# Kernel optimization log

Measured on AMD Instinct MI355X. Metric: run time of the kernel, lower is better.

The kernel has to match this reference:

```python
import jax, jax.numpy as jnp
import numpy as np

B, S, L, D, C_ENC, H = 8, 4096, 77, 1280, 2048, 20
DH = D // H          # 64
SCALE = DH ** -0.5


def setup_inputs() -> dict:
    key = jax.random.key(0)
    ks = jax.random.split(key, 8)
    return {
        "hidden_states": jax.random.normal(ks[0], (B, S, D), jnp.float32),
        "encoder_hidden_states": jax.random.normal(ks[1], (B, L, C_ENC), jnp.float32),
        "region_state": jax.random.uniform(ks[2], (B, S, L), jnp.float32),
        "Wq": jax.random.normal(ks[3], (D, D), jnp.float32) * 0.02,
        "Wk": jax.random.normal(ks[4], (C_ENC, D), jnp.float32) * 0.02,
        "Wv": jax.random.normal(ks[5], (C_ENC, D), jnp.float32) * 0.02,
        "Wo": jax.random.normal(ks[6], (D, D), jnp.float32) * 0.02,
        "bo": jnp.zeros((D,), jnp.float32),
        "sigma": jnp.ones((1,), jnp.float32) * 14.6,
    }


def reference(hidden_states, encoder_hidden_states, region_state, Wq, Wk, Wv, Wo, bo, sigma):
    # QKV projections (dense GEMMs)
    q = (hidden_states @ Wq).reshape(B, S, H, DH)            # [B,S,H,dh]
    k = (encoder_hidden_states @ Wk).reshape(B, L, H, DH)    # [B,L,H,dh]
    v = (encoder_hidden_states @ Wv).reshape(B, L, H, DH)
    # scaled attention scores (baddbmm with beta=0 == plain scaled matmul)
    scores = jnp.einsum('bshd,blhd->bhsl', q, k) * SCALE      # [B,H,S,L]
    # region-prompt bias: weight_func(w, sigma, qk) = w * log(1 + 0.1*sigma) * qk.max()
    # repeat_interleave over heads == broadcast over the head axis
    bias = region_state * (jnp.log1p(sigma[0] * 0.1) * scores.max())  # [B,S,L]
    scores = scores + bias[:, None, :, :]
    probs = jax.nn.softmax(scores, axis=-1)
    out = jnp.einsum('bhsl,blhd->bshd', probs, v).reshape(B, S, D)
    # output projection (to_out[0]); to_out[1] is dropout (identity at eval)
    return out @ Wo + bo
```

## Files before the change

### kernel.cpp

```cpp
#include <hip/hip_runtime.h>
#include <hip/hip_bf16.h>
#include <math.h>

#define NB 8
#define NS 4096
#define NL 77
#define NLP 80
#define NLPV 96
#define ND 1280
#define NC 2048
#define NH 20
#define NDH 64
#define QK_SCALE 0.125f

typedef __attribute__((ext_vector_type(4))) float f32x4;
typedef __attribute__((ext_vector_type(8))) short bf16x8;

static __device__ __forceinline__ void gload_lds16(const void* g, void* l) {
  __builtin_amdgcn_global_load_lds(
      (const __attribute__((address_space(1))) void*)g,
      (__attribute__((address_space(3))) void*)l, 16, 0, 0);
}

#define BAR() do { asm volatile("" ::: "memory"); __builtin_amdgcn_s_barrier(); asm volatile("" ::: "memory"); } while (0)
#define LGKM0() asm volatile("s_waitcnt lgkmcnt(0)" ::: "memory")

__global__ void cvt_bf16_kern(const float* __restrict__ in,
                              __hip_bfloat16* __restrict__ out, long n)
{
  long i = ((long)blockIdx.x * blockDim.x + threadIdx.x) * 4;
  long stride = (long)gridDim.x * blockDim.x * 4;
  for (; i < n; i += stride) {
    float4 v = *reinterpret_cast<const float4*>(in + i);
    union { __hip_bfloat16 h[4]; ushort4 u; } r;
    r.h[0] = __float2bfloat16(v.x);
    r.h[1] = __float2bfloat16(v.y);
    r.h[2] = __float2bfloat16(v.z);
    r.h[3] = __float2bfloat16(v.w);
    *reinterpret_cast<ushort4*>(out + i) = r.u;
  }
}

__global__ void transpose_bf16_kern(const float* __restrict__ in,
                                    __hip_bfloat16* __restrict__ out,
                                    int rows, int cols)
{
  __shared__ float t[32][33];
  int c0 = blockIdx.x * 32, r0 = blockIdx.y * 32;
  int tx = threadIdx.x, ty = threadIdx.y;
  for (int i = ty; i < 32; i += 8) {
    int r = r0 + i, c = c0 + tx;
    t[i][tx] = (r < rows && c < cols) ? in[(long)r * cols + c] : 0.f;
  }
  __syncthreads();
  for (int i = ty; i < 32; i += 8) {
    int oc = c0 + i, orr = r0 + tx;
    if (oc < cols && orr < rows)
      out[(long)oc * rows + orr] = __float2bfloat16(t[tx][i]);
  }
}

__global__ __launch_bounds__(256)
void gemm_bt_kern(const __hip_bfloat16* __restrict__ A,
                  const __hip_bfloat16* __restrict__ Bt,
                  void* __restrict__ C, const float* __restrict__ bias,
                  int M, int N, int K, int mode)
{
  __shared__ __align__(16) __hip_bfloat16 As[128 * 32];
  __shared__ __align__(16) __hip_bfloat16 Bs[128 * 32];
  const int t = threadIdx.x;
  const int lane = t & 63;
  const int w = t >> 6;
  const int wm = w >> 1, wn = w & 1;
  const int lr = lane & 15, hi = lane >> 4, lk = hi * 8;
  const long m0 = (long)blockIdx.x * 128;
  const long n0 = (long)blockIdx.y * 128;

  f32x4 acc[4][4];
#pragma unroll
  for (int mi = 0; mi < 4; ++mi)
#pragma unroll
    for (int ni = 0; ni < 4; ++ni) acc[mi][ni] = {0.f, 0.f, 0.f, 0.f};

  for (int k0 = 0; k0 < K; k0 += 32) {
    __syncthreads();
#pragma unroll
    for (int rnd = 0; rnd < 2; ++rnd) {
      int idx = rnd * 256 + t;
      int row = idx >> 2, kpp = (idx & 3) * 8;
      long arow = m0 + row; if (arow >= M) arow = M - 1;
      gload_lds16(A + arow * K + k0 + kpp, (void*)(As + idx * 8));
      long brow = n0 + row;
      gload_lds16(Bt + brow * K + k0 + kpp, (void*)(Bs + idx * 8));
    }
    __syncthreads();

    bf16x8 af[4], bfr[4];
#pragma unroll
    for (int i = 0; i < 4; ++i) {
      af[i]  = *reinterpret_cast<const bf16x8*>(As + (wm * 64 + i * 16 + lr) * 32 + lk);
      bfr[i] = *reinterpret_cast<const bf16x8*>(Bs + (wn * 64 + i * 16 + lr) * 32 + lk);
    }
#pragma unroll
    for (int mi = 0; mi < 4; ++mi)
#pragma unroll
      for (int ni = 0; ni < 4; ++ni)
        acc[mi][ni] = __builtin_amdgcn_mfma_f32_16x16x32_bf16(af[mi], bfr[ni], acc[mi][ni], 0, 0, 0);
  }

#pragma unroll
  for (int mi = 0; mi < 4; ++mi) {
#pragma unroll
    for (int r = 0; r < 4; ++r) {
      long row = m0 + wm * 64 + mi * 16 + hi * 4 + r;
      if (row < M) {
#pragma unroll
        for (int ni = 0; ni < 4; ++ni) {
          long col = n0 + wn * 64 + ni * 16 + lr;
          if (mode == 0)
            ((__hip_bfloat16*)C)[row * N + col] = __float2bfloat16(acc[mi][ni][r]);
          else
            ((float*)C)[row * N + col] = acc[mi][ni][r] + bias[col];
        }
      }
    }
  }
}

__global__ __launch_bounds__(256, 2)
void gemm_qmax_kern(const __hip_bfloat16* __restrict__ A,
                    const __hip_bfloat16* __restrict__ Bt,
                    __hip_bfloat16* __restrict__ C,
                    const __hip_bfloat16* __restrict__ kp,
                    float* __restrict__ bmax,
                    int M, int N, int K)
{
  __shared__ __align__(16) __hip_bfloat16 sm[32768];
  char* smc = (char*)sm;

  const int t = threadIdx.x, lane = t & 63, w = t >> 6;
  const int wm = w >> 1, wn = w & 1;
  const int lr = lane & 15, hi = lane >> 4;
  const int sw = lr & 7;

  int nwg = gridDim.x;
  int cpx = nwg >> 3;
  int swz = (blockIdx.x & 7) * cpx + (blockIdx.x >> 3);
  int nxt = N >> 7;
  int mt = swz / nxt, ntile = swz - mt * nxt;
  const long m0 = (long)mt * 128, n0 = (long)ntile * 128;

  const int srow  = t >> 3;
  const int skoff = ((t & 7) ^ (srow & 7)) * 8;
  const int sdst  = t * 16;

  f32x4 acc[4][4];
#pragma unroll
  for (int mi = 0; mi < 4; ++mi)
#pragma unroll
    for (int ni = 0; ni < 4; ++ni) acc[mi][ni] = {0.f, 0.f, 0.f, 0.f};

  auto stageA = [&](int b, int kt) {
#pragma unroll
    for (int c = 0; c < 4; ++c)
      gload_lds16(A + (m0 + c * 32 + srow) * (long)K + kt * 64 + skoff,
                  (void*)(smc + b * 16384 + c * 4096 + sdst));
  };
  auto stageB = [&](int b, int kt) {
#pragma unroll
    for (int c = 0; c < 4; ++c)
      gload_lds16(Bt + (n0 + c * 32 + srow) * (long)K + kt * 64 + skoff,
                  (void*)(smc + 32768 + b * 16384 + c * 4096 + sdst));
  };

  const int NT = K >> 6;
  stageA(0, 0); stageB(0, 0);
  stageA(1, 1); stageB(1, 1);
  asm volatile("s_waitcnt vmcnt(8)" ::: "memory");
  BAR();

  for (int t2 = 0; t2 < NT; ++t2) {
    const int b = t2 & 1;
    const char* pa = smc + b * 16384;
    const char* pb = smc + 32768 + b * 16384;
    const bool pf = (t2 + 2 < NT);

    bf16x8 af[4][2], bfr[4][2];
#pragma unroll
    for (int mi = 0; mi < 4; ++mi) {
      int row = wm * 64 + mi * 16 + lr;
#pragma unroll
      for (int kk = 0; kk < 2; ++kk)
        af[mi][kk] = *reinterpret_cast<const bf16x8*>(
            pa + row * 128 + ((((kk * 4 + hi) ^ sw)) << 4));
    }
#pragma unroll
    for (int ni = 0; ni < 4; ++ni) {
      int row = wn * 64 + ni * 16 + lr;
#pragma unroll
      for (int kk = 0; kk < 2; ++kk)
        bfr[ni][kk] = *reinterpret_cast<const bf16x8*>(
            pb + row * 128 + ((((kk * 4 + hi) ^ sw)) << 4));
    }
    __builtin_amdgcn_s_setprio(1);
#pragma unroll
    for (int mi = 0; mi < 4; ++mi)
#pragma unroll
      for (int ni = 0; ni < 4; ++ni) {
        acc[mi][ni] = __builtin_amdgcn_mfma_f32_16x16x32_bf16(af[mi][0], bfr[ni][0], acc[mi][ni], 0, 0, 0);
        acc[mi][ni] = __builtin_amdgcn_mfma_f32_16x16x32_bf16(af[mi][1], bfr[ni][1], acc[mi][ni], 0, 0, 0);
      }
    __builtin_amdgcn_s_setprio(0);

    LGKM0();
    BAR();
    if (pf) { stageA(b, t2 + 2); stageB(b, t2 + 2); }
    if (pf) { asm volatile("s_waitcnt vmcnt(8)" ::: "memory"); }
    else    { asm volatile("s_waitcnt vmcnt(0)" ::: "memory"); }
    BAR();
  }

  __hip_bfloat16* qsl = (__hip_bfloat16*)smc;
#pragma unroll
  for (int mi = 0; mi < 4; ++mi)
#pragma unroll
    for (int r = 0; r < 4; ++r) {
      int rowl = wm * 64 + mi * 16 + hi * 4 + r;
      long row = m0 + rowl;
#pragma unroll
      for (int ni = 0; ni < 4; ++ni) {
        int col = wn * 64 + ni * 16 + lr;
        __hip_bfloat16 v = __float2bfloat16(acc[mi][ni][r]);
        C[row * N + n0 + col] = v;
        int bw = (col >> 3) ^ (rowl & 7);
        qsl[rowl * 128 + (bw << 3) + (col & 7)] = v;
      }
    }
  LGKM0();
  BAR();
  const int bb = (int)(m0 >> 12);
  float mx = -1e30f;
#pragma unroll
  for (int hh = 0; hh < 2; ++hh) {
    const int h = (int)(n0 >> 6) + hh;
    bf16x8 bk0[5], bk1[5];
#pragma unroll
    for (int lt = 0; lt < 5; ++lt) {
      const __hip_bfloat16* Kr = kp + ((long)(bb * NLP + lt * 16 + lr)) * ND + h * NDH + hi * 8;
      bk0[lt] = *reinterpret_cast<const bf16x8*>(Kr);
      bk1[lt] = *reinterpret_cast<const bf16x8*>(Kr + 32);
    }
#pragma unroll
    for (int su = 0; su < 2; ++su) {
      int qrow = (w * 2 + su) * 16 + lr;
      int bi0 = (hh * 8 + hi)     ^ sw;
      int bi1 = (hh * 8 + 4 + hi) ^ sw;
      bf16x8 aq0 = *reinterpret_cast<const bf16x8*>(qsl + qrow * 128 + (bi0 << 3));
      bf16x8 aq1 = *reinterpret_cast<const bf16x8*>(qsl + qrow * 128 + (bi1 << 3));
#pragma unroll
      for (int lt = 0; lt < 5; ++lt) {
        f32x4 sc = {0.f, 0.f, 0.f, 0.f};
        sc = __builtin_amdgcn_mfma_f32_16x16x32_bf16(aq0, bk0[lt], sc, 0, 0, 0);
        sc = __builtin_amdgcn_mfma_f32_16x16x32_bf16(aq1, bk1[lt], sc, 0, 0, 0);
        if ((lt < 4) || (lr < 13)) {
#pragma unroll
          for (int r = 0; r < 4; ++r) mx = fmaxf(mx, sc[r]);
        }
      }
    }
  }
#pragma unroll
  for (int k = 32; k >= 1; k >>= 1) mx = fmaxf(mx, __shfl_xor(mx, k));
  float* wmx = (float*)(smc + 32768);
  if (lane == 0) wmx[w] = mx;
  LGKM0();
  BAR();
  if (t == 0) {
    float mm = fmaxf(fmaxf(wmx[0], wmx[1]), fmaxf(wmx[2], wmx[3]));
    bmax[blockIdx.x] = mm * QK_SCALE;
  }
}

__global__ __launch_bounds__(256, 2)
void gemm_out_kern(const __hip_bfloat16* __restrict__ A,
                   const __hip_bfloat16* __restrict__ Bt,
                   float* __restrict__ C, const float* __restrict__ bias,
                   int M, int N, int K)
{
  __shared__ __align__(16) __hip_bfloat16 sm[32768];
  char* smc = (char*)sm;

  const int t = threadIdx.x, lane = t & 63, w = t >> 6;
  const int wm = w >> 1, wn = w & 1;
  const int lr = lane & 15, hi = lane >> 4;
  const int sw = lr & 7;

  int nwg = gridDim.x;
  int cpx = nwg >> 3;
  int swz = (blockIdx.x & 7) * cpx + (blockIdx.x >> 3);
  int nxt = N >> 7;
  int mt = swz / nxt, ntile = swz - mt * nxt;
  const long m0 = (long)mt * 128, n0 = (long)ntile * 128;

  const int srow  = t >> 3;
  const int skoff = ((t & 7) ^ (srow & 7)) * 8;
  const int sdst  = t * 16;

  f32x4 acc[4][4];
#pragma unroll
  for (int mi = 0; mi < 4; ++mi)
#pragma unroll
    for (int ni = 0; ni < 4; ++ni) acc[mi][ni] = {0.f, 0.f, 0.f, 0.f};

  auto stageA = [&](int b, int kt) {
#pragma unroll
    for (int c = 0; c < 4; ++c)
      gload_lds16(A + (m0 + c * 32 + srow) * (long)K + kt * 64 + skoff,
                  (void*)(smc + b * 16384 + c * 4096 + sdst));
  };
  auto stageB = [&](int b, int kt) {
#pragma unroll
    for (int c = 0; c < 4; ++c)
      gload_lds16(Bt + (n0 + c * 32 + srow) * (long)K + kt * 64 + skoff,
                  (void*)(smc + 32768 + b * 16384 + c * 4096 + sdst));
  };

  const int NT = K >> 6;
  stageA(0, 0); stageB(0, 0);
  stageA(1, 1); stageB(1, 1);
  asm volatile("s_waitcnt vmcnt(8)" ::: "memory");
  BAR();

  for (int t2 = 0; t2 < NT; ++t2) {
    const int b = t2 & 1;
    const char* pa = smc + b * 16384;
    const char* pb = smc + 32768 + b * 16384;
    const bool pf = (t2 + 2 < NT);

    bf16x8 af[4][2], bfr[4][2];
#pragma unroll
    for (int mi = 0; mi < 4; ++mi) {
      int row = wm * 64 + mi * 16 + lr;
#pragma unroll
      for (int kk = 0; kk < 2; ++kk)
        af[mi][kk] = *reinterpret_cast<const bf16x8*>(
            pa + row * 128 + ((((kk * 4 + hi) ^ sw)) << 4));
    }
#pragma unroll
    for (int ni = 0; ni < 4; ++ni) {
      int row = wn * 64 + ni * 16 + lr;
#pragma unroll
      for (int kk = 0; kk < 2; ++kk)
        bfr[ni][kk] = *reinterpret_cast<const bf16x8*>(
            pb + row * 128 + ((((kk * 4 + hi) ^ sw)) << 4));
    }
    __builtin_amdgcn_s_setprio(1);
#pragma unroll
    for (int mi = 0; mi < 4; ++mi)
#pragma unroll
      for (int ni = 0; ni < 4; ++ni) {
        acc[mi][ni] = __builtin_amdgcn_mfma_f32_16x16x32_bf16(af[mi][0], bfr[ni][0], acc[mi][ni], 0, 0, 0);
        acc[mi][ni] = __builtin_amdgcn_mfma_f32_16x16x32_bf16(af[mi][1], bfr[ni][1], acc[mi][ni], 0, 0, 0);
      }
    __builtin_amdgcn_s_setprio(0);

    LGKM0();
    BAR();
    if (pf) { stageA(b, t2 + 2); stageB(b, t2 + 2); }
    if (pf) { asm volatile("s_waitcnt vmcnt(8)" ::: "memory"); }
    else    { asm volatile("s_waitcnt vmcnt(0)" ::: "memory"); }
    BAR();
  }

  float bv[4];
#pragma unroll
  for (int ni = 0; ni < 4; ++ni) bv[ni] = bias[n0 + wn * 64 + ni * 16 + lr];
#pragma unroll
  for (int mi = 0; mi < 4; ++mi)
#pragma unroll
    for (int r = 0; r < 4; ++r) {
      long row = m0 + wm * 64 + mi * 16 + hi * 4 + r;
#pragma unroll
      for (int ni = 0; ni < 4; ++ni) {
        long col = n0 + wn * 64 + ni * 16 + lr;
        C[row * N + col] = acc[mi][ni][r] + bv[ni];
      }
    }
}

__global__ void repack_kv_kern(const __hip_bfloat16* __restrict__ kvc,
                               __hip_bfloat16* __restrict__ kp,
                               __hip_bfloat16* __restrict__ vt)
{
  int idx = blockIdx.x * 256 + threadIdx.x;
  const __hip_bfloat16 z = __float2bfloat16(0.f);
  if (idx < NB * NLP * ND) {
    int d = idx % ND;
    int l = (idx / ND) % NLP;
    int b = idx / (ND * NLP);
    kp[idx] = (l < NL) ? kvc[((long)(b * NL + l)) * 2560 + d] : z;
  }
  if (idx < NB * NH * NDH * NLPV) {
    int l  = idx % NLPV;
    int dh = (idx / NLPV) % NDH;
    int h  = (idx / (NLPV * NDH)) % NH;
    int b  = idx / (NLPV * NDH * NH);
    vt[idx] = (l < NL) ? kvc[((long)(b * NL + l)) * 2560 + ND + h * NDH + dh] : z;
  }
}

__global__ void reduce_max_kern(const float* __restrict__ bm, int n,
                                const float* __restrict__ sigma,
                                float* __restrict__ cb)
{
  __shared__ float sm[256];
  float m = -1e30f;
  for (int i = threadIdx.x; i < n; i += 256) m = fmaxf(m, bm[i]);
  sm[threadIdx.x] = m;
  __syncthreads();
  for (int s = 128; s > 0; s >>= 1) {
    if (threadIdx.x < (unsigned)s) sm[threadIdx.x] = fmaxf(sm[threadIdx.x], sm[threadIdx.x + s]);
    __syncthreads();
  }
  if (threadIdx.x == 0) cb[0] = log1pf(sigma[0] * 0.1f) * sm[0];
}

__global__ __launch_bounds__(256)
void attn_kern(const __hip_bfloat16* __restrict__ qb,
               const __hip_bfloat16* __restrict__ kp,
               const __hip_bfloat16* __restrict__ vt,
               const float* __restrict__ rs,
               const float* __restrict__ cb,
               __hip_bfloat16* __restrict__ ao_out)
{
  __shared__ __align__(16) float rsl[64][80];
  __shared__ __align__(16) __hip_bfloat16 pl[4][16][NLPV];
  int t = threadIdx.x, lane = t & 63, wi = t >> 6;
  int b = blockIdx.y;
  int s0 = blockIdx.x * 64;
  int lr = lane & 15, hi = lane >> 4, lk = hi * 8;
  const float c = cb[0];

  for (int i = t; i < 64 * NL; i += 256) {
    int rr = i / NL, cc = i - rr * NL;
    rsl[rr][cc] = rs[((long)(b * NS + s0 + rr)) * NL + cc] * c;
  }
#pragma unroll
  for (int r = 0; r < 4; ++r)
    pl[wi][hi * 4 + r][80 + lr] = __float2bfloat16(0.f);
  __syncthreads();

  const int rw = wi * 16;
  const __hip_bfloat16* Qrow = qb + ((long)(b * NS + s0 + rw + lr)) * ND;
  const __hip_bfloat16* Krow = kp + ((long)(b * NLP + lr)) * ND;

  for (int h = 0; h < NH; ++h) {
    const __hip_bfloat16* Qp = Qrow + h * NDH + lk;
    bf16x8 aq0 = *reinterpret_cast<const bf16x8*>(Qp);
    bf16x8 aq1 = *reinterpret_cast<const bf16x8*>(Qp + 32);

    f32x4 sc[5];
#pragma unroll
    for (int lt = 0; lt < 5; ++lt) {
      const __hip_bfloat16* Kr = Krow + (long)lt * 16 * ND + h * NDH + lk;
      bf16x8 bk0 = *reinterpret_cast<const bf16x8*>(Kr);
      bf16x8 bk1 = *reinterpret_cast<const bf16x8*>(Kr + 32);
      f32x4 z = {0.f, 0.f, 0.f, 0.f};
      z = __builtin_amdgcn_mfma_f32_16x16x32_bf16(aq0, bk0, z, 0, 0, 0);
      sc[lt] = __builtin_amdgcn_mfma_f32_16x16x32_bf16(aq1, bk1, z, 0, 0, 0);
    }

    float sv[5][4];
    float pm[4] = {-1e30f, -1e30f, -1e30f, -1e30f};
#pragma unroll
    for (int lt = 0; lt < 5; ++lt) {
      int l = lt * 16 + lr;
#pragma unroll
      for (int r = 0; r < 4; ++r) {
        if (l < NL) {
          float v = sc[lt][r] * QK_SCALE + rsl[rw + hi * 4 + r][l];
          sv[lt][r] = v;
          pm[r] = fmaxf(pm[r], v);
        } else {
          sv[lt][r] = -1e30f;
        }
      }
    }
#pragma unroll
    for (int r = 0; r < 4; ++r)
#pragma unroll
      for (int k = 8; k >= 1; k >>= 1) pm[r] = fmaxf(pm[r], __shfl_xor(pm[r], k));

    float p[5][4];
    float psum[4] = {0.f, 0.f, 0.f, 0.f};
#pragma unroll
    for (int lt = 0; lt < 5; ++lt) {
      int l = lt * 16 + lr;
#pragma unroll
      for (int r = 0; r < 4; ++r) {
        float e = (l < NL) ? __expf(sv[lt][r] - pm[r]) : 0.f;
        p[lt][r] = e;
        psum[r] += e;
      }
    }
#pragma unroll
    for (int r = 0; r < 4; ++r)
#pragma unroll
      for (int k = 8; k >= 1; k >>= 1) psum[r] += __shfl_xor(psum[r], k);
    float rinv[4];
#pragma unroll
    for (int r = 0; r < 4; ++r) rinv[r] = 1.f / psum[r];

    LGKM0();

#pragma unroll
    for (int lt = 0; lt < 5; ++lt)
#pragma unroll
      for (int r = 0; r < 4; ++r)
        pl[wi][hi * 4 + r][lt * 16 + lr] = __float2bfloat16(p[lt][r]);

    LGKM0();

    f32x4 ao[4];
#pragma unroll
    for (int nt = 0; nt < 4; ++nt) ao[nt] = {0.f, 0.f, 0.f, 0.f};
    const __hip_bfloat16* Vb = vt + ((long)((b * NH + h) * NDH)) * NLPV;
#pragma unroll
    for (int ks = 0; ks < 3; ++ks) {
      bf16x8 pa = *reinterpret_cast<const bf16x8*>(&pl[wi][lr][ks * 32 + lk]);
#pragma unroll
      for (int nt = 0; nt < 4; ++nt) {
        bf16x8 bv = *reinterpret_cast<const bf16x8*>(Vb + ((long)(nt * 16 + lr)) * NLPV + ks * 32 + lk);
        ao[nt] = __builtin_amdgcn_mfma_f32_16x16x32_bf16(pa, bv, ao[nt], 0, 0, 0);
      }
    }

#pragma unroll
    for (int nt = 0; nt < 4; ++nt)
#pragma unroll
      for (int r = 0; r < 4; ++r) {
        int srow = s0 + rw + hi * 4 + r;
        ao_out[((long)(b * NS + srow)) * ND + h * NDH + nt * 16 + lr] =
            __float2bfloat16(ao[nt][r] * rinv[r]);
      }
  }
}

extern "C" void kernel_launch(void* const* d_in, const int* in_sizes, int n_in,
                              void* d_out, int out_size, void* d_ws, size_t ws_size,
                              hipStream_t stream)
{
  const float* hs    = (const float*)d_in[0];
  const float* ehs   = (const float*)d_in[1];
  const float* rs    = (const float*)d_in[2];
  const float* Wq    = (const float*)d_in[3];
  const float* Wk    = (const float*)d_in[4];
  const float* Wv    = (const float*)d_in[5];
  const float* Wo    = (const float*)d_in[6];
  const float* bo    = (const float*)d_in[7];
  const float* sigma = (const float*)d_in[8];
  float* out = (float*)d_out;

  char* ws = (char*)d_ws;
  size_t off = 0;
  auto alloc = [&](size_t bytes) {
    void* p = ws + off;
    off = (off + bytes + 255) & ~(size_t)255;
    return p;
  };
  __hip_bfloat16* hsb  = (__hip_bfloat16*)alloc((size_t)NB * NS * ND * 2);
  __hip_bfloat16* qb   = (__hip_bfloat16*)alloc((size_t)NB * NS * ND * 2);
  __hip_bfloat16* wqt  = (__hip_bfloat16*)alloc((size_t)ND * ND * 2);
  __hip_bfloat16* wkvt = (__hip_bfloat16*)alloc((size_t)2560 * NC * 2);
  __hip_bfloat16* wot  = (__hip_bfloat16*)alloc((size_t)ND * ND * 2);
  __hip_bfloat16* ehsb = (__hip_bfloat16*)alloc((size_t)NB * NL * NC * 2);
  __hip_bfloat16* kvc  = (__hip_bfloat16*)alloc((size_t)NB * NL * 2560 * 2);
  __hip_bfloat16* kp   = (__hip_bfloat16*)alloc((size_t)NB * NLP * ND * 2);
  __hip_bfloat16* vt   = (__hip_bfloat16*)alloc((size_t)NB * NH * NDH * NLPV * 2);
  float* bmax = (float*)alloc(10240 * 4);
  float* cb   = (float*)alloc(256);

  cvt_bf16_kern<<<2048, 256, 0, stream>>>(hs, hsb, (long)NB * NS * ND);
  cvt_bf16_kern<<<512, 256, 0, stream>>>(ehs, ehsb, (long)NB * NL * NC);

  transpose_bf16_kern<<<dim3(40, 40), dim3(32, 8), 0, stream>>>(Wq, wqt, ND, ND);
  transpose_bf16_kern<<<dim3(40, 64), dim3(32, 8), 0, stream>>>(Wk, wkvt, NC, ND);
  transpose_bf16_kern<<<dim3(40, 64), dim3(32, 8), 0, stream>>>(Wv, wkvt + (size_t)ND * NC, NC, ND);
  transpose_bf16_kern<<<dim3(40, 40), dim3(32, 8), 0, stream>>>(Wo, wot, ND, ND);

  gemm_bt_kern<<<dim3(5, 20), 256, 0, stream>>>(ehsb, wkvt, kvc, nullptr, NB * NL, 2560, NC, 0);
  repack_kv_kern<<<3840, 256, 0, stream>>>(kvc, kp, vt);

  gemm_qmax_kern<<<2560, 256, 0, stream>>>(hsb, wqt, qb, kp, bmax, NB * NS, ND, ND);

  reduce_max_kern<<<1, 256, 0, stream>>>(bmax, 2560, sigma, cb);

  attn_kern<<<dim3(NS / 64, NB), 256, 0, stream>>>(qb, kp, vt, rs, cb, hsb);

  gemm_out_kern<<<2560, 256, 0, stream>>>(hsb, wot, out, bo, NB * NS, ND, ND);
}
```

Baseline: 484.5 us.

## Fuse prep kernels, write K/V directly from GEMM, halve GEMM K-tile for occupancy

The six conversion and transpose launches are merged into one prep kernel. The KV GEMM epilogue now writes straight into the padded K and transposed V layouts, which removes the intermediate buffer and the repack kernel; padding comes from two memsets instead. The Q and output GEMMs drop from a 64 to a 32 K-tile with an unswizzled LDS layout, halving shared memory so launch bounds can request 4 blocks per SIMD instead of 2. The risks are more loop iterations and barriers per GEMM, possible LDS bank conflicts from the simpler layout, and register pressure at the higher occupancy.

Measured after the change: 634.4 us. 1.31x slower.

```diff
diff --git a/kernel.cpp b/kernel.cpp
--- a/kernel.cpp
+++ b/kernel.cpp
@@ -25,46 +25,61 @@
 #define BAR() do { asm volatile("" ::: "memory"); __builtin_amdgcn_s_barrier(); asm volatile("" ::: "memory"); } while (0)
 #define LGKM0() asm volatile("s_waitcnt lgkmcnt(0)" ::: "memory")
 
-__global__ void cvt_bf16_kern(const float* __restrict__ in,
-                              __hip_bfloat16* __restrict__ out, long n)
-{
-  long i = ((long)blockIdx.x * blockDim.x + threadIdx.x) * 4;
-  long stride = (long)gridDim.x * blockDim.x * 4;
-  for (; i < n; i += stride) {
-    float4 v = *reinterpret_cast<const float4*>(in + i);
-    union { __hip_bfloat16 h[4]; ushort4 u; } r;
-    r.h[0] = __float2bfloat16(v.x);
-    r.h[1] = __float2bfloat16(v.y);
-    r.h[2] = __float2bfloat16(v.z);
-    r.h[3] = __float2bfloat16(v.w);
-    *reinterpret_cast<ushort4*>(out + i) = r.u;
-  }
-}
-
-__global__ void transpose_bf16_kern(const float* __restrict__ in,
-                                    __hip_bfloat16* __restrict__ out,
-                                    int rows, int cols)
-{
-  __shared__ float t[32][33];
-  int c0 = blockIdx.x * 32, r0 = blockIdx.y * 32;
-  int tx = threadIdx.x, ty = threadIdx.y;
+__global__ __launch_bounds__(256)
+void prep_kern(const float* __restrict__ hs,  __hip_bfloat16* __restrict__ hsb,
+               const float* __restrict__ ehs, __hip_bfloat16* __restrict__ ehsb,
+               const float* __restrict__ Wq,  __hip_bfloat16* __restrict__ wqt,
+               const float* __restrict__ Wk,  const float* __restrict__ Wv,
+               __hip_bfloat16* __restrict__ wkvt,
+               const float* __restrict__ Wo,  __hip_bfloat16* __restrict__ wot)
+{
+  const int bid = blockIdx.x, t = threadIdx.x;
+  if (bid < 2560) {
+    const float* in; __hip_bfloat16* outp; long n; long i; long stride;
+    if (bid < 2048) {
+      in = hs; outp = hsb; n = (long)NB * NS * ND;
+      i = ((long)bid * 256 + t) * 4; stride = 2048L * 256 * 4;
+    } else {
+      in = ehs; outp = ehsb; n = (long)NB * NL * NC;
+      i = ((long)(bid - 2048) * 256 + t) * 4; stride = 512L * 256 * 4;
+    }
+    for (; i < n; i += stride) {
+      float4 v = *reinterpret_cast<const float4*>(in + i);
+      union { __hip_bfloat16 h[4]; ushort4 u; } r;
+      r.h[0] = __float2bfloat16(v.x);
+      r.h[1] = __float2bfloat16(v.y);
+      r.h[2] = __float2bfloat16(v.z);
+      r.h[3] = __float2bfloat16(v.w);
+      *reinterpret_cast<ushort4*>(outp + i) = r.u;
+    }
+    return;
+  }
+  __shared__ float tl[32][33];
+  const float* in; __hip_bfloat16* outp; int rows, cols, idx;
+  if (bid < 4160)      { idx = bid - 2560; in = Wq; outp = wqt; rows = 1280; cols = 1280; }
+  else if (bid < 6720) { idx = bid - 4160; in = Wk; outp = wkvt; rows = 2048; cols = 1280; }
+  else if (bid < 9280) { idx = bid - 6720; in = Wv; outp = wkvt + (size_t)ND * NC; rows = 2048; cols = 1280; }
+  else                 { idx = bid - 9280; in = Wo; outp = wot; rows = 1280; cols = 1280; }
+  int c0 = (idx % 40) * 32, r0 = (idx / 40) * 32;
+  int tx = t & 31, ty = t >> 5;
   for (int i = ty; i < 32; i += 8) {
     int r = r0 + i, c = c0 + tx;
-    t[i][tx] = (r < rows && c < cols) ? in[(long)r * cols + c] : 0.f;
+    tl[i][tx] = (r < rows && c < cols) ? in[(long)r * cols + c] : 0.f;
   }
   __syncthreads();
   for (int i = ty; i < 32; i += 8) {
     int oc = c0 + i, orr = r0 + tx;
     if (oc < cols && orr < rows)
-      out[(long)oc * rows + orr] = __float2bfloat16(t[tx][i]);
+      outp[(long)oc * rows + orr] = __float2bfloat16(tl[tx][i]);
   }
 }
 
 __global__ __launch_bounds__(256)
-void gemm_bt_kern(const __hip_bfloat16* __restrict__ A,
+void gemm_kv_kern(const __hip_bfloat16* __restrict__ A,
                   const __hip_bfloat16* __restrict__ Bt,
-                  void* __restrict__ C, const float* __restrict__ bias,
-                  int M, int N, int K, int mode)
+                  __hip_bfloat16* __restrict__ kp,
+                  __hip_bfloat16* __restrict__ vt,
+                  int M, int N, int K)
 {
   __shared__ __align__(16) __hip_bfloat16 As[128 * 32];
   __shared__ __align__(16) __hip_bfloat16 Bs[128 * 32];
@@ -114,20 +129,24 @@
     for (int r = 0; r < 4; ++r) {
       long row = m0 + wm * 64 + mi * 16 + hi * 4 + r;
       if (row < M) {
+        int b = (int)(row / NL), l = (int)(row - (long)b * NL);
 #pragma unroll
         for (int ni = 0; ni < 4; ++ni) {
           long col = n0 + wn * 64 + ni * 16 + lr;
-          if (mode == 0)
-            ((__hip_bfloat16*)C)[row * N + col] = __float2bfloat16(acc[mi][ni][r]);
-          else
-            ((float*)C)[row * N + col] = acc[mi][ni][r] + bias[col];
+          __hip_bfloat16 v = __float2bfloat16(acc[mi][ni][r]);
+          if (col < ND) {
+            kp[((long)(b * NLP + l)) * ND + col] = v;
+          } else {
+            int c2 = (int)(col - ND);
+            vt[(((long)(b * NH + (c2 >> 6))) * NDH + (c2 & 63)) * NLPV + l] = v;
+          }
         }
       }
     }
   }
 }
 
-__global__ __launch_bounds__(256, 2)
+__global__ __launch_bounds__(256, 4)
 void gemm_qmax_kern(const __hip_bfloat16* __restrict__ A,
                     const __hip_bfloat16* __restrict__ Bt,
                     __hip_bfloat16* __restrict__ C,
@@ -135,7 +154,8 @@
                     float* __restrict__ bmax,
                     int M, int N, int K)
 {
-  __shared__ __align__(16) __hip_bfloat16 sm[32768];
+  __shared__ __align__(16) __hip_bfloat16 sm[16384];
+  __shared__ float wmx[4];
   char* smc = (char*)sm;
 
   const int t = threadIdx.x, lane = t & 63, w = t >> 6;
@@ -150,9 +170,8 @@
   int mt = swz / nxt, ntile = swz - mt * nxt;
   const long m0 = (long)mt * 128, n0 = (long)ntile * 128;
 
-  const int srow  = t >> 3;
-  const int skoff = ((t & 7) ^ (srow & 7)) * 8;
-  const int sdst  = t * 16;
+  const int g_row = w * 16 + lr;
+  const int g_k   = hi * 8;
 
   f32x4 acc[4][4];
 #pragma unroll
@@ -162,60 +181,49 @@
 
   auto stageA = [&](int b, int kt) {
 #pragma unroll
-    for (int c = 0; c < 4; ++c)
-      gload_lds16(A + (m0 + c * 32 + srow) * (long)K + kt * 64 + skoff,
-                  (void*)(smc + b * 16384 + c * 4096 + sdst));
+    for (int c = 0; c < 2; ++c)
+      gload_lds16(A + (m0 + c * 64 + g_row) * (long)K + kt * 32 + g_k,
+                  (void*)(smc + b * 8192 + c * 4096 + t * 16));
   };
   auto stageB = [&](int b, int kt) {
 #pragma unroll
-    for (int c = 0; c < 4; ++c)
-      gload_lds16(Bt + (n0 + c * 32 + srow) * (long)K + kt * 64 + skoff,
-                  (void*)(smc + 32768 + b * 16384 + c * 4096 + sdst));
+    for (int c = 0; c < 2; ++c)
+      gload_lds16(Bt + (n0 + c * 64 + g_row) * (long)K + kt * 32 + g_k,
+                  (void*)(smc + 16384 + b * 8192 + c * 4096 + t * 16));
   };
 
-  const int NT = K >> 6;
+  const int NT = K >> 5;
   stageA(0, 0); stageB(0, 0);
   stageA(1, 1); stageB(1, 1);
-  asm volatile("s_waitcnt vmcnt(8)" ::: "memory");
+  asm volatile("s_waitcnt vmcnt(4)" ::: "memory");
   BAR();
 
   for (int t2 = 0; t2 < NT; ++t2) {
     const int b = t2 & 1;
-    const char* pa = smc + b * 16384;
-    const char* pb = smc + 32768 + b * 16384;
+    const char* pa = smc + b * 8192;
+    const char* pb = smc + 16384 + b * 8192;
     const bool pf = (t2 + 2 < NT);
 
-    bf16x8 af[4][2], bfr[4][2];
-#pragma unroll
-    for (int mi = 0; mi < 4; ++mi) {
-      int row = wm * 64 + mi * 16 + lr;
-#pragma unroll
-      for (int kk = 0; kk < 2; ++kk)
-        af[mi][kk] = *reinterpret_cast<const bf16x8*>(
-            pa + row * 128 + ((((kk * 4 + hi) ^ sw)) << 4));
-    }
-#pragma unroll
-    for (int ni = 0; ni < 4; ++ni) {
-      int row = wn * 64 + ni * 16 + lr;
-#pragma unroll
-      for (int kk = 0; kk < 2; ++kk)
-        bfr[ni][kk] = *reinterpret_cast<const bf16x8*>(
-            pb + row * 128 + ((((kk * 4 + hi) ^ sw)) << 4));
-    }
+    bf16x8 af[4], bfr[4];
+#pragma unroll
+    for (int mi = 0; mi < 4; ++mi)
+      af[mi] = *reinterpret_cast<const bf16x8*>(pa + (wm * 4 + mi) * 1024 + hi * 256 + lr * 16);
+#pragma unroll
+    for (int ni = 0; ni < 4; ++ni)
+      bfr[ni] = *reinterpret_cast<const bf16x8*>(pb + (wn * 4 + ni) * 1024 + hi * 256 + lr * 16);
+
     __builtin_amdgcn_s_setprio(1);
 #pragma unroll
     for (int mi = 0; mi < 4; ++mi)
 #pragma unroll
-      for (int ni = 0; ni < 4; ++ni) {
-        acc[mi][ni] = __builtin_amdgcn_mfma_f32_16x16x32_bf16(af[mi][0], bfr[ni][0], acc[mi][ni], 0, 0, 0);
-        acc[mi][ni] = __builtin_amdgcn_mfma_f32_16x16x32_bf16(af[mi][1], bfr[ni][1], acc[mi][ni], 0, 0, 0);
-      }
+      for (int ni = 0; ni < 4; ++ni)
+        acc[mi][ni] = __builtin_amdgcn_mfma_f32_16x16x32_bf16(af[mi], bfr[ni], acc[mi][ni], 0, 0, 0);
     __builtin_amdgcn_s_setprio(0);
 
     LGKM0();
     BAR();
     if (pf) { stageA(b, t2 + 2); stageB(b, t2 + 2); }
-    if (pf) { asm volatile("s_waitcnt vmcnt(8)" ::: "memory"); }
+    if (pf) { asm volatile("s_waitcnt vmcnt(4)" ::: "memory"); }
     else    { asm volatile("s_waitcnt vmcnt(0)" ::: "memory"); }
     BAR();
   }
@@ -271,7 +279,6 @@
   }
 #pragma unroll
   for (int k = 32; k >= 1; k >>= 1) mx = fmaxf(mx, __shfl_xor(mx, k));
-  float* wmx = (float*)(smc + 32768);
   if (lane == 0) wmx[w] = mx;
   LGKM0();
   BAR();
@@ -281,19 +288,18 @@
   }
 }
 
-__global__ __launch_bounds__(256, 2)
+__global__ __launch_bounds__(256, 4)
 void gemm_out_kern(const __hip_bfloat16* __restrict__ A,
                    const __hip_bfloat16* __restrict__ Bt,
                    float* __restrict__ C, const float* __restrict__ bias,
                    int M, int N, int K)
 {
-  __shared__ __align__(16) __hip_bfloat16 sm[32768];
+  __shared__ __align__(16) __hip_bfloat16 sm[16384];
   char* smc = (char*)sm;
 
   const int t = threadIdx.x, lane = t & 63, w = t >> 6;
   const int wm = w >> 1, wn = w & 1;
   const int lr = lane & 15, hi = lane >> 4;
-  const int sw = lr & 7;
 
   int nwg = gridDim.x;
   int cpx = nwg >> 3;
@@ -302,9 +308,8 @@
   int mt = swz / nxt, ntile = swz - mt * nxt;
   const long m0 = (long)mt * 128, n0 = (long)ntile * 128;
 
-  const int srow  = t >> 3;
-  const int skoff = ((t & 7) ^ (srow & 7)) * 8;
-  const int sdst  = t * 16;
+  const int g_row = w * 16 + lr;
+  const int g_k   = hi * 8;
 
   f32x4 acc[4][4];
 #pragma unroll
@@ -314,60 +319,49 @@
 
   auto stageA = [&](int b, int kt) {
 #pragma unroll
-    for (int c = 0; c < 4; ++c)
-      gload_lds16(A + (m0 + c * 32 + srow) * (long)K + kt * 64 + skoff,
-                  (void*)(smc + b * 16384 + c * 4096 + sdst));
+    for (int c = 0; c < 2; ++c)
+      gload_lds16(A + (m0 + c * 64 + g_row) * (long)K + kt * 32 + g_k,
+                  (void*)(smc + b * 8192 + c * 4096 + t * 16));
   };
   auto stageB = [&](int b, int kt) {
 #pragma unroll
-    for (int c = 0; c < 4; ++c)
-      gload_lds16(Bt + (n0 + c * 32 + srow) * (long)K + kt * 64 + skoff,
-                  (void*)(smc + 32768 + b * 16384 + c * 4096 + sdst));
+    for (int c = 0; c < 2; ++c)
+      gload_lds16(Bt + (n0 + c * 64 + g_row) * (long)K + kt * 32 + g_k,
+                  (void*)(smc + 16384 + b * 8192 + c * 4096 + t * 16));
   };
 
-  const int NT = K >> 6;
+  const int NT = K >> 5;
   stageA(0, 0); stageB(0, 0);
   stageA(1, 1); stageB(1, 1);
-  asm volatile("s_waitcnt vmcnt(8)" ::: "memory");
+  asm volatile("s_waitcnt vmcnt(4)" ::: "memory");
   BAR();
 
   for (int t2 = 0; t2 < NT; ++t2) {
     const int b = t2 & 1;
-    const char* pa = smc + b * 16384;
-    const char* pb = smc + 32768 + b * 16384;
+    const char* pa = smc + b * 8192;
+    const char* pb = smc + 16384 + b * 8192;
     const bool pf = (t2 + 2 < NT);
 
-    bf16x8 af[4][2], bfr[4][2];
-#pragma unroll
-    for (int mi = 0; mi < 4; ++mi) {
-      int row = wm * 64 + mi * 16 + lr;
-#pragma unroll
-      for (int kk = 0; kk < 2; ++kk)
-        af[mi][kk] = *reinterpret_cast<const bf16x8*>(
-            pa + row * 128 + ((((kk * 4 + hi) ^ sw)) << 4));
-    }
-#pragma unroll
-    for (int ni = 0; ni < 4; ++ni) {
-      int row = wn * 64 + ni * 16 + lr;
-#pragma unroll
-      for (int kk = 0; kk < 2; ++kk)
-        bfr[ni][kk] = *reinterpret_cast<const bf16x8*>(
-            pb + row * 128 + ((((kk * 4 + hi) ^ sw)) << 4));
-    }
+    bf16x8 af[4], bfr[4];
+#pragma unroll
+    for (int mi = 0; mi < 4; ++mi)
+      af[mi] = *reinterpret_cast<const bf16x8*>(pa + (wm * 4 + mi) * 1024 + hi * 256 + lr * 16);
+#pragma unroll
+    for (int ni = 0; ni < 4; ++ni)
+      bfr[ni] = *reinterpret_cast<const bf16x8*>(pb + (wn * 4 + ni) * 1024 + hi * 256 + lr * 16);
+
     __builtin_amdgcn_s_setprio(1);
 #pragma unroll
     for (int mi = 0; mi < 4; ++mi)
 #pragma unroll
-      for (int ni = 0; ni < 4; ++ni) {
-        acc[mi][ni] = __builtin_amdgcn_mfma_f32_16x16x32_bf16(af[mi][0], bfr[ni][0], acc[mi][ni], 0, 0, 0);
-        acc[mi][ni] = __builtin_amdgcn_mfma_f32_16x16x32_bf16(af[mi][1], bfr[ni][1], acc[mi][ni], 0, 0, 0);
-      }
+      for (int ni = 0; ni < 4; ++ni)
+        acc[mi][ni] = __builtin_amdgcn_mfma_f32_16x16x32_bf16(af[mi], bfr[ni], acc[mi][ni], 0, 0, 0);
     __builtin_amdgcn_s_setprio(0);
 
     LGKM0();
     BAR();
     if (pf) { stageA(b, t2 + 2); stageB(b, t2 + 2); }
-    if (pf) { asm volatile("s_waitcnt vmcnt(8)" ::: "memory"); }
+    if (pf) { asm volatile("s_waitcnt vmcnt(4)" ::: "memory"); }
     else    { asm volatile("s_waitcnt vmcnt(0)" ::: "memory"); }
     BAR();
   }
@@ -386,27 +380,6 @@
         C[row * N + col] = acc[mi][ni][r] + bv[ni];
       }
     }
-}
-
-__global__ void repack_kv_kern(const __hip_bfloat16* __restrict__ kvc,
-                               __hip_bfloat16* __restrict__ kp,
-                               __hip_bfloat16* __restrict__ vt)
-{
-  int idx = blockIdx.x * 256 + threadIdx.x;
-  const __hip_bfloat16 z = __float2bfloat16(0.f);
-  if (idx < NB * NLP * ND) {
-    int d = idx % ND;
-    int l = (idx / ND) % NLP;
-    int b = idx / (ND * NLP);
-    kp[idx] = (l < NL) ? kvc[((long)(b * NL + l)) * 2560 + d] : z;
-  }
-  if (idx < NB * NH * NDH * NLPV) {
-    int l  = idx % NLPV;
-    int dh = (idx / NLPV) % NDH;
-    int h  = (idx / (NLPV * NDH)) % NH;
-    int b  = idx / (NLPV * NDH * NH);
-    vt[idx] = (l < NL) ? kvc[((long)(b * NL + l)) * 2560 + ND + h * NDH + dh] : z;
-  }
 }
 
 __global__ void reduce_max_kern(const float* __restrict__ bm, int n,
@@ -574,22 +547,17 @@
   __hip_bfloat16* wkvt = (__hip_bfloat16*)alloc((size_t)2560 * NC * 2);
   __hip_bfloat16* wot  = (__hip_bfloat16*)alloc((size_t)ND * ND * 2);
   __hip_bfloat16* ehsb = (__hip_bfloat16*)alloc((size_t)NB * NL * NC * 2);
-  __hip_bfloat16* kvc  = (__hip_bfloat16*)alloc((size_t)NB * NL * 2560 * 2);
   __hip_bfloat16* kp   = (__hip_bfloat16*)alloc((size_t)NB * NLP * ND * 2);
   __hip_bfloat16* vt   = (__hip_bfloat16*)alloc((size_t)NB * NH * NDH * NLPV * 2);
   float* bmax = (float*)alloc(10240 * 4);
   float* cb   = (float*)alloc(256);
 
-  cvt_bf16_kern<<<2048, 256, 0, stream>>>(hs, hsb, (long)NB * NS * ND);
-  cvt_bf16_kern<<<512, 256, 0, stream>>>(ehs, ehsb, (long)NB * NL * NC);
-
-  transpose_bf16_kern<<<dim3(40, 40), dim3(32, 8), 0, stream>>>(Wq, wqt, ND, ND);
-  transpose_bf16_kern<<<dim3(40, 64), dim3(32, 8), 0, stream>>>(Wk, wkvt, NC, ND);
-  transpose_bf16_kern<<<dim3(40, 64), dim3(32, 8), 0, stream>>>(Wv, wkvt + (size_t)ND * NC, NC, ND);
-  transpose_bf16_kern<<<dim3(40, 40), dim3(32, 8), 0, stream>>>(Wo, wot, ND, ND);
-
-  gemm_bt_kern<<<dim3(5, 20), 256, 0, stream>>>(ehsb, wkvt, kvc, nullptr, NB * NL, 2560, NC, 0);
-  repack_kv_kern<<<3840, 256, 0, stream>>>(kvc, kp, vt);
+  hipMemsetAsync(kp, 0, (size_t)NB * NLP * ND * 2, stream);
+  hipMemsetAsync(vt, 0, (size_t)NB * NH * NDH * NLPV * 2, stream);
+
+  prep_kern<<<10880, 256, 0, stream>>>(hs, hsb, ehs, ehsb, Wq, wqt, Wk, Wv, wkvt, Wo, wot);
+
+  gemm_kv_kern<<<dim3(5, 20), 256, 0, stream>>>(ehsb, wkvt, kp, vt, NB * NL, 2560, NC);
 
   gemm_qmax_kern<<<2560, 256, 0, stream>>>(hsb, wqt, qb, kp, bmax, NB * NS, ND, ND);
 
```
